# Kernel optimization log

Hardware: AMD Instinct MI355X
Metric: run time of the kernel (lower is better)

Reference implementation:

```python
import jax, jax.numpy as jnp
import numpy as np

BATCH, NUM_BSS, NUM_USERS, M, N = 32, 8, 32, 128, 4
LAGR_ITERS = 8
PSEUDOINV_SVAL_THRESH = 1e-12


def herm(a):
    return 0.5 * (a + jnp.swapaxes(a, -1, -2).conj())


def setup_inputs() -> dict:
    key = jax.random.key(0)
    ks = jax.random.split(key, 7)
    v_re = jax.random.normal(ks[0], (BATCH, NUM_USERS, M, N), jnp.float32)
    v_im = jax.random.normal(ks[1], (BATCH, NUM_USERS, M, N), jnp.float32)
    H_re = jax.random.normal(ks[2], (NUM_BSS, NUM_USERS, N, M), jnp.float32)
    H_im = jax.random.normal(ks[3], (NUM_BSS, NUM_USERS, N, M), jnp.float32)
    noise_pow = jax.random.uniform(ks[4], (BATCH, NUM_USERS), jnp.float32, 0.05, 1.0)
    rweights = jax.random.uniform(ks[5], (BATCH, NUM_USERS), jnp.float32, 0.1, 1.0)
    bss_pow = jnp.ones((BATCH, NUM_BSS), jnp.float32)
    assign = jax.random.randint(ks[6], (NUM_USERS,), 0, NUM_BSS).astype(jnp.int32)
    return {"v_re": v_re, "v_im": v_im, "H_re": H_re, "H_im": H_im,
            "noise_pow": noise_pow, "rweights": rweights, "bss_pow": bss_pow,
            "assign": assign}


def reference(v_re, v_im, H_re, H_im, noise_pow, rweights, bss_pow, assign):
    V = v_re + 1j * v_im          # [B,K,M,N] precoders
    H = H_re + 1j * H_im          # [C,K,N,M] channel BS c -> user k
    K = V.shape[1]
    C = H.shape[0]
    Ndim = V.shape[-1]
    eyeN = jnp.eye(Ndim, dtype=V.dtype)

    # Hg[j, i] = channel from assigned-BS-of-user-j to user i
    Hg = H[assign]                                    # [K,K,N,M]
    # downlink covariance per user i: noise*I + sum_j (H[bs_j,i] V_j)(.)^H
    HV = jnp.einsum('jinm,bjmp->bijnp', Hg, V)        # [B,Ki,Kj,N,N]
    cov = jnp.einsum('bijnp,bijqp->binq', HV, HV.conj())
    cov = herm(cov + noise_pow[..., None, None] * eyeN)
    icov = herm(jnp.linalg.inv(cov))                  # [B,K,N,N]

    idx = jnp.arange(K)
    Hd = Hg[idx, idx]                                 # [K,N,M] direct channels
    HdV = jnp.einsum('knm,bkmp->bknp', Hd, V)         # [B,K,N,N]
    u = jnp.einsum('bknq,bkqp->bknp', icov, HdV)      # receive filters
    w_inv = herm(eyeN - jnp.einsum('bkqn,bkqp->bknp', u.conj(), HdV))
    w = herm(jnp.linalg.inv(w_inv))                   # MSE weights (w_poly=None)
    uwu = herm(jnp.einsum('bknp,bkpq,bkrq->bknr', u, w, u.conj()))
    # v_tilde = H_ii^H u w * rate_weight
    vt = jnp.einsum('knm,bknp,bkpq->bkmq', Hd.conj(), u, w) * rweights[..., None, None]

    # uplink covariance per BS c: sum_k rw_k * H[c,k]^H uwu_k H[c,k]
    ul = herm(jnp.einsum('cknm,bkno,ckop,bk->bcmp', H.conj(), uwu, H, rweights))

    # aux per BS: sum over assigned users of v_tilde v_tilde^H
    Q = jnp.einsum('bkmn,bkpn->bkmp', vt, vt.conj())  # [B,K,M,M]
    aux = jnp.moveaxis(
        jax.ops.segment_sum(jnp.moveaxis(Q, 1, 0), assign, num_segments=C), 0, 1)  # [B,C,M,M]

    lam, E = jnp.linalg.eigh(ul)                      # [B,C,M], [B,C,M,M]
    lam = jnp.maximum(lam, 0.0)
    c = jnp.maximum(jnp.einsum('bcmi,bcmp,bcpi->bci', E.conj(), aux, E).real, 0.0)
    c = c / bss_pow[..., None]

    # solve sum_i c_i/(lam_i+mu)^2 = 1 for mu >= 0 by bisection in [0, sqrt(sum c)]
    hi = jnp.sqrt(jnp.sum(c, -1))
    lo = jnp.zeros_like(hi)
    for _ in range(LAGR_ITERS):
        mid = 0.5 * (lo + hi)
        f = jnp.sum(c / jnp.square(lam + mid[..., None] + 1e-20), -1)
        gt = f > 1.0
        lo = jnp.where(gt, mid, lo)
        hi = jnp.where(gt, hi, mid)
    mu = jnp.maximum(0.5 * (lo + hi), 0.0)            # [B,C]

    # pseudo-inverse of loaded UL covariance via its eigendecomposition
    lam_l = lam + mu[..., None]
    lam_l = jnp.where(lam_l < PSEUDOINV_SVAL_THRESH, 1e12, lam_l)
    inv_aug = herm(jnp.einsum('bcmi,bci,bcni->bcmn', E, 1.0 / lam_l, E.conj()))

    # v update: v_k = inv_aug[assign_k] @ v_tilde_k
    v_out = jnp.einsum('bkmp,bkpn->bkmn', inv_aug[:, assign], vt)  # [B,K,M,N]
    return v_out
```

## Files before the change

### kernel.cpp

```cpp
#include <hip/hip_runtime.h>

#define B_ 32
#define C_ 8
#define K_ 32
#define NCMAX 96
#define BSTR 129

__device__ __forceinline__ float2 cmul(float2 a, float2 b) {
  return make_float2(a.x*b.x - a.y*b.y, a.x*b.y + a.y*b.x);
}
__device__ __forceinline__ float2 cmulc(float2 a, float2 b) {
  return make_float2(a.x*b.x + a.y*b.y, a.y*b.x - a.x*b.y);
}
__device__ __forceinline__ float2 cadd(float2 a, float2 b){ return make_float2(a.x+b.x, a.y+b.y); }
__device__ __forceinline__ float2 csub(float2 a, float2 b){ return make_float2(a.x-b.x, a.y-b.y); }
__device__ __forceinline__ int SK(int r){ return r + ((r >> 3) << 1); }

__device__ void herm4_inv(float2 a[4][4], float2 out[4][4]) {
  float idg[4];
  for (int j = 0; j < 4; ++j) {
    float d = sqrtf(fmaxf(a[j][j].x, 1e-30f));
    float id = 1.f / d;
    idg[j] = id;
    a[j][j] = make_float2(d, 0.f);
    for (int r = j+1; r < 4; ++r) { a[r][j].x *= id; a[r][j].y *= id; }
    for (int c = j+1; c < 4; ++c)
      for (int r = c; r < 4; ++r)
        a[r][c] = csub(a[r][c], cmulc(a[r][j], a[c][j]));
  }
  float2 li[4][4];
  for (int j = 0; j < 4; ++j) {
    li[j][j] = make_float2(idg[j], 0.f);
    for (int r = j+1; r < 4; ++r) {
      float2 s = make_float2(0.f, 0.f);
      for (int d = j; d < r; ++d) s = cadd(s, cmul(a[r][d], li[d][j]));
      li[r][j] = make_float2(-s.x*idg[r], -s.y*idg[r]);
    }
  }
  for (int p = 0; p < 4; ++p)
    for (int q = 0; q < 4; ++q) {
      float2 s = make_float2(0.f, 0.f);
      for (int d = (p > q ? p : q); d < 4; ++d)
        s = cadd(s, cmulc(li[d][q], li[d][p]));
      out[p][q] = s;
    }
}

__global__ __launch_bounds__(512, 1) void k_fused(
    const float* __restrict__ v_re, const float* __restrict__ v_im,
    const float* __restrict__ H_re, const float* __restrict__ H_im,
    const float* __restrict__ noise_pow, const float* __restrict__ rweights,
    const float* __restrict__ bss_pow, const int* __restrict__ assign_g,
    void* __restrict__ outp, int omode)
{
  const int t = threadIdx.x;
  const int lane = t & 63, wid = t >> 6;
  const int blk = blockIdx.x;
  const int b = blk >> 3, c = blk & 7;
  const int tm = t >> 4, tp = t & 15;
  const int rbase = tm * 4, cbase = tp * 8;

  __shared__ __align__(16) float2 Bs[NCMAX * BSTR];
  __shared__ __align__(16) float2 Arena[4224];
  __shared__ __align__(16) float2 Vp[16 * 128];
  __shared__ __align__(16) float2 pS[1024];
  __shared__ __align__(16) float2 colS[160];
  __shared__ __align__(16) float2 pvS[160];
  __shared__ __align__(16) float2 tauS[128];
  __shared__ float dS[128], eS[128], cpS[128];
  __shared__ float red[8];
  __shared__ int asg[K_], ulist[K_], nc_s;

  float2* Wall = pS;
  float2* uwS  = pS + 512;
  float2* covS = Arena + 2576;
  float2* HdVS = Arena + 3088;
  float2* Hs   = Arena;
  float2* Ys   = Arena + 520;
  float2* Tsc  = Arena;

  if (t < K_) asg[t] = assign_g[t];
  if (t == 0) {
    int n2 = 0;
    for (int k = 0; k < K_; ++k) if (assign_g[k] == c) ulist[n2++] = k;
    nc_s = n2;
  }
  {
    const int k = t >> 4, n = (t >> 2) & 3, q = t & 3;
    covS[t] = make_float2((n == q) ? noise_pow[b*K_ + k] : 0.f, 0.f);
  }
  __syncthreads();
  const int nc = nc_s;
  if (nc == 0) return;
  const int cols = 4 * nc;
  const int passes = (cols + 31) >> 5;

  {
    const int pn = t >> 2, qt = t & 3;
    const int kk = pn >> 2, nn = pn & 3;
    float2* Tb0 = Arena + 1552;
    float2* Tb1 = Arena + 2064;
    for (int j = 0; j < K_; j += 2) {
      #pragma unroll
      for (int bf = 0; bf < 2; ++bf) {
        const int vb = (b*K_ + j + bf) * 512;
        Arena[bf*776 + (t >> 2)*6 + (t & 3) + (t >> 7)*2] =
            make_float2(v_re[vb + t], v_im[vb + t]);
      }
      __syncthreads();
      float2 rr[2][4];
      #pragma unroll
      for (int bf = 0; bf < 2; ++bf) {
        const float2* Vq = Arena + bf*776 + qt*2;
        const int hb = ((asg[j + bf]*K_ + kk)*4 + nn) * 128;
        float2 a0 = {0,0}, a1 = {0,0}, a2 = {0,0}, a3 = {0,0};
        for (int m4 = qt*32; m4 < qt*32 + 32; m4 += 4) {
          const float4 hre = *(const float4*)&H_re[hb + m4];
          const float4 him = *(const float4*)&H_im[hb + m4];
          const float hx[4] = {hre.x, hre.y, hre.z, hre.w};
          const float hy[4] = {him.x, him.y, him.z, him.w};
          #pragma unroll
          for (int i2 = 0; i2 < 4; ++i2) {
            const float4 v01 = *(const float4*)&Vq[(m4 + i2)*6];
            const float4 v23 = *(const float4*)&Vq[(m4 + i2)*6 + 2];
            a0.x += hx[i2]*v01.x - hy[i2]*v01.y; a0.y += hx[i2]*v01.y + hy[i2]*v01.x;
            a1.x += hx[i2]*v01.z - hy[i2]*v01.w; a1.y += hx[i2]*v01.w + hy[i2]*v01.z;
            a2.x += hx[i2]*v23.x - hy[i2]*v23.y; a2.y += hx[i2]*v23.y + hy[i2]*v23.x;
            a3.x += hx[i2]*v23.z - hy[i2]*v23.w; a3.y += hx[i2]*v23.w + hy[i2]*v23.z;
          }
        }
        rr[bf][0] = a0; rr[bf][1] = a1; rr[bf][2] = a2; rr[bf][3] = a3;
      }
      #pragma unroll
      for (int o = 1; o <= 2; o <<= 1) {
        #pragma unroll
        for (int bf = 0; bf < 2; ++bf)
          #pragma unroll
          for (int p = 0; p < 4; ++p) {
            rr[bf][p].x += __shfl_xor(rr[bf][p].x, o, 64);
            rr[bf][p].y += __shfl_xor(rr[bf][p].y, o, 64);
          }
      }
      if (qt == 0) {
        #pragma unroll
        for (int p = 0; p < 4; ++p) {
          Tb0[pn*4 + p] = rr[0][p];
          Tb1[pn*4 + p] = rr[1][p];
        }
      }
      __syncthreads();
      {
        const int k2 = t >> 4, n2 = (t >> 2) & 3, q2 = t & 3;
        float2 acc = covS[t];
        #pragma unroll
        for (int p = 0; p < 4; ++p)
          acc = cadd(acc, cmulc(Tb0[(k2*4 + n2)*4 + p], Tb0[(k2*4 + q2)*4 + p]));
        #pragma unroll
        for (int p = 0; p < 4; ++p)
          acc = cadd(acc, cmulc(Tb1[(k2*4 + n2)*4 + p], Tb1[(k2*4 + q2)*4 + p]));
        covS[t] = acc;
        if (k2 == j)     HdVS[k2*16 + n2*4 + q2] = Tb0[(k2*4 + n2)*4 + q2];
        if (k2 == j + 1) HdVS[k2*16 + n2*4 + q2] = Tb1[(k2*4 + n2)*4 + q2];
      }
      __syncthreads();
    }
  }

  if (t < K_) {
    const int k = t;
    float2 a[4][4], ic[4][4], hv[4][4], u[4][4], wi[4][4], w[4][4], uw[4][4], W[4][4];
    const float rwk = rweights[b*K_ + k];
    for (int r = 0; r < 4; ++r)
      for (int c2 = 0; c2 < 4; ++c2) a[r][c2] = covS[k*16 + r*4 + c2];
    herm4_inv(a, ic);
    for (int r = 0; r < 4; ++r)
      for (int c2 = 0; c2 < 4; ++c2) hv[r][c2] = HdVS[k*16 + r*4 + c2];
    for (int n = 0; n < 4; ++n)
      for (int p = 0; p < 4; ++p) {
        float2 s = {0,0};
        for (int q = 0; q < 4; ++q) s = cadd(s, cmul(ic[n][q], hv[q][p]));
        u[n][p] = s;
      }
    for (int n = 0; n < 4; ++n)
      for (int p = 0; p < 4; ++p) {
        float2 s = make_float2((n == p) ? 1.f : 0.f, 0.f);
        for (int q = 0; q < 4; ++q) s = csub(s, cmulc(hv[q][p], u[q][n]));
        wi[n][p] = s;
      }
    herm4_inv(wi, w);
    for (int n = 0; n < 4; ++n)
      for (int q = 0; q < 4; ++q) {
        float2 s = {0,0};
        for (int p = 0; p < 4; ++p) s = cadd(s, cmul(u[n][p], w[p][q]));
        uw[n][q] = s;
      }
    for (int n = 0; n < 4; ++n)
      for (int r = 0; r < 4; ++r) {
        float2 s = {0,0};
        for (int q = 0; q < 4; ++q) s = cadd(s, cmulc(uw[n][q], u[r][q]));
        W[n][r] = make_float2(s.x * rwk, s.y * rwk);
      }
    for (int n = 0; n < 4; ++n)
      for (int r = n; r < 4; ++r) {
        float2 x1 = W[n][r], x2 = W[r][n];
        float2 hm = make_float2(0.5f*(x1.x + x2.x), 0.5f*(x1.y - x2.y));
        W[n][r] = hm; W[r][n] = make_float2(hm.x, -hm.y);
      }
    for (int idx = 0; idx < 16; ++idx) {
      uwS[k*16 + idx]  = uw[idx >> 2][idx & 3];
      Wall[k*16 + idx] = W[idx >> 2][idx & 3];
    }
  }
  __syncthreads();

  float trp = 0.f;
  #pragma unroll
  for (int q = 0; q < 8; ++q) {
    const int col = tp + 16*q;
    const int slot = col >> 2, qn = col & 3;
    if (slot < nc) {
      const int k = ulist[slot];
      const float rwk = rweights[b*K_ + k];
      const int hb = (c*K_ + k) * 512;
      float2 acc0 = {0,0}, acc1 = {0,0}, acc2 = {0,0}, acc3 = {0,0};
      #pragma unroll
      for (int n = 0; n < 4; ++n) {
        const float2 uwv = uwS[k*16 + n*4 + qn];
        const float4 hre = *(const float4*)&H_re[hb + n*128 + rbase];
        const float4 him = *(const float4*)&H_im[hb + n*128 + rbase];
        acc0 = cadd(acc0, cmulc(uwv, make_float2(hre.x, him.x)));
        acc1 = cadd(acc1, cmulc(uwv, make_float2(hre.y, him.y)));
        acc2 = cadd(acc2, cmulc(uwv, make_float2(hre.z, him.z)));
        acc3 = cadd(acc3, cmulc(uwv, make_float2(hre.w, him.w)));
      }
      acc0.x *= rwk; acc0.y *= rwk; acc1.x *= rwk; acc1.y *= rwk;
      acc2.x *= rwk; acc2.y *= rwk; acc3.x *= rwk; acc3.y *= rwk;
      Bs[col*BSTR + rbase]     = acc0;
      Bs[col*BSTR + rbase + 1] = acc1;
      Bs[col*BSTR + rbase + 2] = acc2;
      Bs[col*BSTR + rbase + 3] = acc3;
      trp += acc0.x*acc0.x + acc0.y*acc0.y + acc1.x*acc1.x + acc1.y*acc1.y
           + acc2.x*acc2.x + acc2.y*acc2.y + acc3.x*acc3.x + acc3.y*acc3.y;
    }
  }
  #pragma unroll
  for (int o = 32; o >= 1; o >>= 1) trp += __shfl_xor(trp, o, 64);
  if (lane == 0) red[wid] = trp;
  __syncthreads();
  const float inv_bss = 1.f / bss_pow[b*C_ + c];
  float hi = sqrtf((red[0] + red[1] + red[2] + red[3] +
                    red[4] + red[5] + red[6] + red[7]) * inv_bss);
  float lo = 0.f;

  float2 Areg[4][8];
  #pragma unroll
  for (int j = 0; j < 4; ++j)
    #pragma unroll
    for (int cc = 0; cc < 8; ++cc) Areg[j][cc] = make_float2(0.f, 0.f);
  __syncthreads();
  for (int k = 0; k < K_; ++k) {
    const int hb = (c*K_ + k) * 512;
    Hs[(t >> 7)*130 + (t & 127)] = make_float2(H_re[hb + t], H_im[hb + t]);
    __syncthreads();
    {
      const int n = t >> 7, p = t & 127;
      float2 y = {0,0};
      #pragma unroll
      for (int o = 0; o < 4; ++o) y = cadd(y, cmul(Wall[k*16 + n*4 + o], Hs[o*130 + p]));
      Ys[n*160 + p + ((p >> 3) << 1)] = y;
    }
    __syncthreads();
    #pragma unroll
    for (int n = 0; n < 4; ++n) {
      float2 h[4], y[8];
      {
        const float4 ha = *(const float4*)&Hs[n*130 + rbase];
        const float4 hc = *(const float4*)&Hs[n*130 + rbase + 2];
        h[0] = make_float2(ha.x, ha.y); h[1] = make_float2(ha.z, ha.w);
        h[2] = make_float2(hc.x, hc.y); h[3] = make_float2(hc.z, hc.w);
        const float2* yb = &Ys[n*160 + tp*10];
        #pragma unroll
        for (int a2 = 0; a2 < 8; a2 += 2) {
          const float4 y4 = *(const float4*)&yb[a2];
          y[a2] = make_float2(y4.x, y4.y); y[a2+1] = make_float2(y4.z, y4.w);
        }
      }
      #pragma unroll
      for (int j = 0; j < 4; ++j)
        #pragma unroll
        for (int cc = 0; cc < 8; ++cc) {
          Areg[j][cc].x += h[j].x*y[cc].x + h[j].y*y[cc].y;
          Areg[j][cc].y += h[j].x*y[cc].y - h[j].y*y[cc].x;
        }
    }
    __syncthreads();
  }

  if (tp == 0) {
    #pragma unroll
    for (int j = 0; j < 4; ++j) colS[SK(rbase + j)] = Areg[j][0];
  }
  __syncthreads();

  #pragma unroll 1
  for (int i = 0; i < 127; ++i) {
    float2 vr[4], vc[8], tau, sc;
    const int slot = (i & 15) << 7;
    {
      const float2 x0 = colS[SK(lane)], x1 = colS[SK(lane + 64)];
      float sig = 0.f;
      if (lane >= i + 2)      sig += x0.x*x0.x + x0.y*x0.y;
      if (lane + 64 >= i + 2) sig += x1.x*x1.x + x1.y*x1.y;
      #pragma unroll
      for (int o = 32; o >= 1; o >>= 1) sig += __shfl_xor(sig, o, 64);
      const float2 al = colS[SK(i + 1)];
      float beta;
      if (sig <= 1e-30f && fabsf(al.y) <= 1e-30f) {
        beta = al.x; tau = make_float2(0.f, 0.f); sc = make_float2(0.f, 0.f);
      } else {
        const float mag = sqrtf(al.x*al.x + al.y*al.y + sig);
        beta = (al.x >= 0.f) ? -mag : mag;
        const float ib = 1.f / beta;
        tau = make_float2((beta - al.x) * ib, -al.y * ib);
        const float dx = al.x - beta, dy = al.y;
        const float dn = 1.f / (dx*dx + dy*dy);
        sc = make_float2(dx*dn, -dy*dn);
      }
      if (t == 0) { eS[i] = beta; tauS[i] = tau; }
      #pragma unroll
      for (int j = 0; j < 4; ++j) {
        const int r = rbase + j;
        const float2 x = colS[SK(r)];
        vr[j] = (r <= i) ? make_float2(0.f, 0.f)
              : (r == i + 1 ? make_float2(1.f, 0.f) : cmul(x, sc));
      }
      {
        const int cb = SK(cbase);
        const float4 c01 = *(const float4*)&colS[cb];
        const float4 c23 = *(const float4*)&colS[cb + 2];
        const float4 c45 = *(const float4*)&colS[cb + 4];
        const float4 c67 = *(const float4*)&colS[cb + 6];
        const float2 cx[8] = { make_float2(c01.x,c01.y), make_float2(c01.z,c01.w),
                               make_float2(c23.x,c23.y), make_float2(c23.z,c23.w),
                               make_float2(c45.x,c45.y), make_float2(c45.z,c45.w),
                               make_float2(c67.x,c67.y), make_float2(c67.z,c67.w) };
        #pragma unroll
        for (int cc = 0; cc < 8; ++cc) {
          const int r = cbase + cc;
          vc[cc] = (r <= i) ? make_float2(0.f, 0.f)
                 : (r == i + 1 ? make_float2(1.f, 0.f) : cmul(cx[cc], sc));
        }
      }
      if (tp == 0) {
        #pragma unroll
        for (int j = 0; j < 4; ++j) Vp[slot + rbase + j] = vr[j];
      }
      float2 part[4];
      #pragma unroll
      for (int j = 0; j < 4; ++j) {
        float2 s = cmul(Areg[j][0], vc[0]);
        #pragma unroll
        for (int cc = 1; cc < 8; ++cc) s = cadd(s, cmul(Areg[j][cc], vc[cc]));
        part[j] = s;
      }
      #pragma unroll
      for (int o = 1; o <= 8; o <<= 1) {
        #pragma unroll
        for (int j = 0; j < 4; ++j) {
          part[j].x += __shfl_xor(part[j].x, o, 64);
          part[j].y += __shfl_xor(part[j].y, o, 64);
        }
      }
      #pragma unroll
      for (int j = 0; j < 4; ++j) if (tp == j) pvS[SK(rbase + j)] = part[j];
    }
    __syncthreads();

    {
      float2 p0 = make_float2(0.f, 0.f), p1 = make_float2(0.f, 0.f);
      if (lane > i)      p0 = cmul(tau, pvS[SK(lane)]);
      if (lane + 64 > i) p1 = cmul(tau, pvS[SK(lane + 64)]);
      const float2 v0 = Vp[slot + lane];
      const float2 v1 = Vp[slot + lane + 64];
      float2 d0 = cadd(cmulc(p0, v0), cmulc(p1, v1));
      #pragma unroll
      for (int o = 32; o >= 1; o >>= 1) {
        d0.x += __shfl_xor(d0.x, o, 64);
        d0.y += __shfl_xor(d0.y, o, 64);
      }
      const float alr = -0.5f * (tau.x*d0.x + tau.y*d0.y);
      float2 wr[4];
      #pragma unroll
      for (int j = 0; j < 4; ++j) {
        const int r = rbase + j;
        float2 p = (r > i) ? cmul(tau, pvS[SK(r)]) : make_float2(0.f, 0.f);
        wr[j] = make_float2(p.x + alr*vr[j].x, p.y + alr*vr[j].y);
      }
      #pragma unroll
      for (int cc = 0; cc < 8; ++cc) {
        const int r = cbase + cc;
        float2 p = (r > i) ? cmul(tau, pvS[SK(r)]) : make_float2(0.f, 0.f);
        const float2 wcv = make_float2(p.x + alr*vc[cc].x, p.y + alr*vc[cc].y);
        #pragma unroll
        for (int j = 0; j < 4; ++j)
          Areg[j][cc] = csub(Areg[j][cc], cadd(cmulc(vr[j], wcv), cmulc(wr[j], vc[cc])));
      }
      if (tp == (i >> 3)) {
        #pragma unroll
        for (int cc = 0; cc < 8; ++cc) if (cc == (i & 7)) {
          #pragma unroll
          for (int j = 0; j < 4; ++j) if (rbase + j >= i + 1) Areg[j][cc] = vr[j];
        }
      }
      if (tp == ((i + 1) >> 3)) {
        #pragma unroll
        for (int cc = 0; cc < 8; ++cc) if (cc == ((i + 1) & 7)) {
          #pragma unroll
          for (int j = 0; j < 4; ++j) colS[SK(rbase + j)] = Areg[j][cc];
        }
      }
    }
    __syncthreads();

    if ((i & 15) == 15 || i == 126) {
      const int p0i = i & ~15;
      const int smax = i - p0i;
      for (int base = 0; base < cols; base += 32) {
        float2 z0[4], z1[4];
        bool act[4];
        #pragma unroll
        for (int qq = 0; qq < 4; ++qq) {
          const int col = base + wid + 8*qq;
          act[qq] = (col < cols);
          const int cc2 = act[qq] ? col : 0;
          z0[qq] = Bs[cc2*BSTR + lane];
          z1[qq] = Bs[cc2*BSTR + lane + 64];
        }
        for (int s = 0; s <= smax; ++s) {
          const float2 tv = tauS[p0i + s];
          const float2 tc = make_float2(tv.x, -tv.y);
          const float2 v0 = Vp[(s << 7) + lane];
          const float2 v1 = Vp[(s << 7) + lane + 64];
          float2 d[4];
          #pragma unroll
          for (int qq = 0; qq < 4; ++qq)
            d[qq] = cadd(cmulc(z0[qq], v0), cmulc(z1[qq], v1));
          #pragma unroll
          for (int o = 32; o >= 1; o >>= 1) {
            #pragma unroll
            for (int qq = 0; qq < 4; ++qq) {
              d[qq].x += __shfl_xor(d[qq].x, o, 64);
              d[qq].y += __shfl_xor(d[qq].y, o, 64);
            }
          }
          #pragma unroll
          for (int qq = 0; qq < 4; ++qq) {
            const float2 td = cmul(tc, d[qq]);
            z0[qq] = csub(z0[qq], cmul(td, v0));
            z1[qq] = csub(z1[qq], cmul(td, v1));
          }
        }
        #pragma unroll
        for (int qq = 0; qq < 4; ++qq) if (act[qq]) {
          const int col = base + wid + 8*qq;
          Bs[col*BSTR + lane]      = z0[qq];
          Bs[col*BSTR + lane + 64] = z1[qq];
        }
      }
      __syncthreads();
    }
  }

  #pragma unroll
  for (int j = 0; j < 4; ++j) {
    const int r = rbase + j;
    if (tp == (r >> 3)) {
      #pragma unroll
      for (int cc = 0; cc < 8; ++cc) if (cc == (r & 7)) dS[r] = Areg[j][cc].x;
    }
  }
  __syncthreads();

  if (wid == 0) {
    for (int it = 0; it <= 8; ++it) {
      const float mu = 0.5f * (lo + hi);
      float fsum = 0.f;
      for (int p = 0; p < passes; ++p) {
        const int colg = 32*p + (lane & 31);
        const bool act = (lane < 32) && (colg < cols);
        float2* Bcol = Bs + colg*BSTR;
        float m = dS[0] + mu;
        float im = 1.f / m;
        float2 g = act ? Bcol[0] : make_float2(0.f, 0.f);
        g.x *= im; g.y *= im;
        if (act) Tsc[lane] = g;
        float cp = eS[0] * im;
        if (lane == 0) cpS[0] = cp;
        for (int r = 1; r < 128; ++r) {
          const float e0 = eS[r-1];
          m = dS[r] + mu - e0 * cp;
          im = 1.f / m;
          float2 gr = act ? Bcol[r] : make_float2(0.f, 0.f);
          gr.x = (gr.x - e0 * g.x) * im;
          gr.y = (gr.y - e0 * g.y) * im;
          g = gr;
          if (act) Tsc[r*33 + lane] = gr;
          if (r < 127) { cp = eS[r] * im; if (lane == 0) cpS[r] = cp; }
        }
        float2 z = g;
        float acc = z.x*z.x + z.y*z.y;
        if (it == 8 && act) Bcol[127] = z;
        for (int r = 126; r >= 0; --r) {
          const float cpr = cpS[r];
          const float2 gp = act ? Tsc[r*33 + lane] : make_float2(0.f, 0.f);
          z.x = gp.x - cpr * z.x;
          z.y = gp.y - cpr * z.y;
          acc += z.x*z.x + z.y*z.y;
          if (it == 8 && act) Bcol[r] = z;
        }
        if (act) fsum += acc;
      }
      if (it < 8) {
        #pragma unroll
        for (int o = 32; o >= 1; o >>= 1) fsum += __shfl_xor(fsum, o, 64);
        const float f = fsum * inv_bss;
        if (f > 1.0f) lo = mu; else hi = mu;
      }
    }
  }
  __syncthreads();

  for (int base = 0; base < cols; base += 32) {
    float2 z0[4], z1[4];
    bool act[4];
    #pragma unroll
    for (int qq = 0; qq < 4; ++qq) {
      const int col = base + wid + 8*qq;
      act[qq] = (col < cols);
      const int cc2 = act[qq] ? col : 0;
      z0[qq] = Bs[cc2*BSTR + lane];
      z1[qq] = Bs[cc2*BSTR + lane + 64];
    }
    for (int P = 7; P >= 0; --P) {
      const int p0i = P * 16;
      const int smax = (P == 7) ? 14 : 15;
      __syncthreads();
      if (tp == 2*P) {
        #pragma unroll
        for (int s = 0; s < 8; ++s) {
          const int ii = p0i + s;
          #pragma unroll
          for (int j = 0; j < 4; ++j) {
            const int r = rbase + j;
            Vp[(s << 7) + r] = (r >= ii + 1) ? Areg[j][s] : make_float2(0.f, 0.f);
          }
        }
      }
      if (tp == 2*P + 1) {
        #pragma unroll
        for (int s = 8; s < 16; ++s) {
          if (s > smax) continue;
          const int ii = p0i + s;
          #pragma unroll
          for (int j = 0; j < 4; ++j) {
            const int r = rbase + j;
            Vp[(s << 7) + r] = (r >= ii + 1) ? Areg[j][s - 8] : make_float2(0.f, 0.f);
          }
        }
      }
      __syncthreads();
      for (int s = smax; s >= 0; --s) {
        const float2 tv = tauS[p0i + s];
        const float2 v0 = Vp[(s << 7) + lane];
        const float2 v1 = Vp[(s << 7) + lane + 64];
        float2 d[4];
        #pragma unroll
        for (int qq = 0; qq < 4; ++qq)
          d[qq] = cadd(cmulc(z0[qq], v0), cmulc(z1[qq], v1));
        #pragma unroll
        for (int o = 32; o >= 1; o >>= 1) {
          #pragma unroll
          for (int qq = 0; qq < 4; ++qq) {
            d[qq].x += __shfl_xor(d[qq].x, o, 64);
            d[qq].y += __shfl_xor(d[qq].y, o, 64);
          }
        }
        #pragma unroll
        for (int qq = 0; qq < 4; ++qq) {
          const float2 td = cmul(tv, d[qq]);
          z0[qq] = csub(z0[qq], cmul(td, v0));
          z1[qq] = csub(z1[qq], cmul(td, v1));
        }
      }
    }
    #pragma unroll
    for (int qq = 0; qq < 4; ++qq) if (act[qq]) {
      const int col = base + wid + 8*qq;
      const int slotc = col >> 2, qn = col & 3;
      const int k = ulist[slotc];
      const size_t obase = (size_t)(b*K_ + k) * 512;
      const size_t oe0 = obase + (size_t)lane*4 + qn;
      const size_t oe1 = obase + (size_t)(lane + 64)*4 + qn;
      if (omode == 0) {
        ((float2*)outp)[oe0] = z0[qq];
        ((float2*)outp)[oe1] = z1[qq];
      } else {
        ((float*)outp)[oe0] = z0[qq].x;
        ((float*)outp)[oe1] = z1[qq].x;
      }
    }
  }
}

extern "C" void kernel_launch(void* const* d_in, const int* in_sizes, int n_in,
                              void* d_out, int out_size, void* d_ws, size_t ws_size,
                              hipStream_t stream)
{
  (void)in_sizes; (void)n_in; (void)d_ws; (void)ws_size;
  const float* v_re   = (const float*)d_in[0];
  const float* v_im   = (const float*)d_in[1];
  const float* H_re   = (const float*)d_in[2];
  const float* H_im   = (const float*)d_in[3];
  const float* noise  = (const float*)d_in[4];
  const float* rw     = (const float*)d_in[5];
  const float* bss    = (const float*)d_in[6];
  const int*   assign = (const int*)d_in[7];

  const int omode = (out_size == B_*K_*128*4) ? 1 : 0;

  hipLaunchKernelGGL(k_fused, dim3(B_*C_), dim3(512), 0, stream,
                     v_re, v_im, H_re, H_im, noise, rw, bss, assign, d_out, omode);
}
```

Baseline: 1.472 ms.

## Apply Householder reflections to B in registers during tridiagonalization

The right-hand-side matrix B now lives in per-thread registers (Bv) and each Householder reflector is applied to it on every step through a cross-thread partial-product reduction in shared memory. This replaces the blocked every-16-steps application that went through a stored Vp panel and wavefront shuffles. The w vector is built once by wave 0 and read from shared memory instead of being recomputed per thread. The A accumulation loop is also moved earlier and processes two users per sync. The costs are extra register pressure, an added reduction and barrier on every iteration, and Vp now aliasing Arena.

Result: faster. 1.354 ms (-8.0%).

```diff
diff --git a/kernel.cpp b/kernel.cpp
--- a/kernel.cpp
+++ b/kernel.cpp
@@ -60,12 +60,13 @@
   const int tm = t >> 4, tp = t & 15;
   const int rbase = tm * 4, cbase = tp * 8;
 
-  __shared__ __align__(16) float2 Bs[NCMAX * BSTR];
+  __shared__ __align__(16) float2 BsL[NCMAX * BSTR];
   __shared__ __align__(16) float2 Arena[4224];
-  __shared__ __align__(16) float2 Vp[16 * 128];
   __shared__ __align__(16) float2 pS[1024];
+  __shared__ __align__(16) float2 dBS2[256];
+  __shared__ __align__(16) float2 wS[160];
   __shared__ __align__(16) float2 colS[160];
-  __shared__ __align__(16) float2 pvS[160];
+  __shared__ __align__(16) float2 pvS[128];
   __shared__ __align__(16) float2 tauS[128];
   __shared__ float dS[128], eS[128], cpS[128];
   __shared__ float red[8];
@@ -75,9 +76,9 @@
   float2* uwS  = pS + 512;
   float2* covS = Arena + 2576;
   float2* HdVS = Arena + 3088;
-  float2* Hs   = Arena;
-  float2* Ys   = Arena + 520;
+  float2* Pd   = Arena;
   float2* Tsc  = Arena;
+  float2* Vp   = Arena;
 
   if (t < K_) asg[t] = assign_g[t];
   if (t == 0) {
@@ -93,6 +94,7 @@
   const int nc = nc_s;
   if (nc == 0) return;
   const int cols = 4 * nc;
+  const int qmax = (cols + 15) >> 4;
   const int passes = (cols + 31) >> 5;
 
   {
@@ -213,6 +215,71 @@
   }
   __syncthreads();
 
+  float2 Areg[4][8];
+  #pragma unroll
+  for (int j = 0; j < 4; ++j)
+    #pragma unroll
+    for (int cc = 0; cc < 8; ++cc) Areg[j][cc] = make_float2(0.f, 0.f);
+  for (int k = 0; k < K_; k += 2) {
+    #pragma unroll
+    for (int bf = 0; bf < 2; ++bf) {
+      const int hb = (c*K_ + k + bf) * 512;
+      Arena[bf*520 + (t >> 7)*130 + (t & 127)] = make_float2(H_re[hb + t], H_im[hb + t]);
+    }
+    __syncthreads();
+    #pragma unroll
+    for (int bf = 0; bf < 2; ++bf) {
+      const int n = t >> 7, p = t & 127;
+      const float2* HsB = Arena + bf*520;
+      const int kb = (k + bf)*16 + n*4;
+      float2 y = {0,0};
+      #pragma unroll
+      for (int o = 0; o < 4; ++o) y = cadd(y, cmul(Wall[kb + o], HsB[o*130 + p]));
+      Arena[1040 + bf*640 + n*160 + p + ((p >> 3) << 1)] = y;
+    }
+    __syncthreads();
+    #pragma unroll
+    for (int bf = 0; bf < 2; ++bf) {
+      const float2* HsB = Arena + bf*520;
+      const float2* YsB = Arena + 1040 + bf*640;
+      #pragma unroll
+      for (int n = 0; n < 4; ++n) {
+        const float4 ha = *(const float4*)&HsB[n*130 + rbase];
+        const float4 hc = *(const float4*)&HsB[n*130 + rbase + 2];
+        const float2 h0 = make_float2(ha.x, ha.y), h1 = make_float2(ha.z, ha.w);
+        const float2 h2 = make_float2(hc.x, hc.y), h3 = make_float2(hc.z, hc.w);
+        const float2* yb = &YsB[n*160 + tp*10];
+        #pragma unroll
+        for (int hq = 0; hq < 2; ++hq) {
+          float2 y[4];
+          #pragma unroll
+          for (int a2 = 0; a2 < 4; a2 += 2) {
+            const float4 y4 = *(const float4*)&yb[hq*4 + a2];
+            y[a2] = make_float2(y4.x, y4.y); y[a2+1] = make_float2(y4.z, y4.w);
+          }
+          #pragma unroll
+          for (int c4 = 0; c4 < 4; ++c4) {
+            const int cc = hq*4 + c4;
+            Areg[0][cc].x += h0.x*y[c4].x + h0.y*y[c4].y;
+            Areg[0][cc].y += h0.x*y[c4].y - h0.y*y[c4].x;
+            Areg[1][cc].x += h1.x*y[c4].x + h1.y*y[c4].y;
+            Areg[1][cc].y += h1.x*y[c4].y - h1.y*y[c4].x;
+            Areg[2][cc].x += h2.x*y[c4].x + h2.y*y[c4].y;
+            Areg[2][cc].y += h2.x*y[c4].y - h2.y*y[c4].x;
+            Areg[3][cc].x += h3.x*y[c4].x + h3.y*y[c4].y;
+            Areg[3][cc].y += h3.x*y[c4].y - h3.y*y[c4].x;
+          }
+        }
+      }
+    }
+    __syncthreads();
+  }
+
+  float2 Bv[4][8];
+  #pragma unroll
+  for (int j = 0; j < 4; ++j)
+    #pragma unroll
+    for (int q = 0; q < 8; ++q) Bv[j][q] = make_float2(0.f, 0.f);
   float trp = 0.f;
   #pragma unroll
   for (int q = 0; q < 8; ++q) {
@@ -235,10 +302,7 @@
       }
       acc0.x *= rwk; acc0.y *= rwk; acc1.x *= rwk; acc1.y *= rwk;
       acc2.x *= rwk; acc2.y *= rwk; acc3.x *= rwk; acc3.y *= rwk;
-      Bs[col*BSTR + rbase]     = acc0;
-      Bs[col*BSTR + rbase + 1] = acc1;
-      Bs[col*BSTR + rbase + 2] = acc2;
-      Bs[col*BSTR + rbase + 3] = acc3;
+      Bv[0][q] = acc0; Bv[1][q] = acc1; Bv[2][q] = acc2; Bv[3][q] = acc3;
       trp += acc0.x*acc0.x + acc0.y*acc0.y + acc1.x*acc1.x + acc1.y*acc1.y
            + acc2.x*acc2.x + acc2.y*acc2.y + acc3.x*acc3.x + acc3.y*acc3.y;
     }
@@ -252,50 +316,6 @@
                     red[4] + red[5] + red[6] + red[7]) * inv_bss);
   float lo = 0.f;
 
-  float2 Areg[4][8];
-  #pragma unroll
-  for (int j = 0; j < 4; ++j)
-    #pragma unroll
-    for (int cc = 0; cc < 8; ++cc) Areg[j][cc] = make_float2(0.f, 0.f);
-  __syncthreads();
-  for (int k = 0; k < K_; ++k) {
-    const int hb = (c*K_ + k) * 512;
-    Hs[(t >> 7)*130 + (t & 127)] = make_float2(H_re[hb + t], H_im[hb + t]);
-    __syncthreads();
-    {
-      const int n = t >> 7, p = t & 127;
-      float2 y = {0,0};
-      #pragma unroll
-      for (int o = 0; o < 4; ++o) y = cadd(y, cmul(Wall[k*16 + n*4 + o], Hs[o*130 + p]));
-      Ys[n*160 + p + ((p >> 3) << 1)] = y;
-    }
-    __syncthreads();
-    #pragma unroll
-    for (int n = 0; n < 4; ++n) {
-      float2 h[4], y[8];
-      {
-        const float4 ha = *(const float4*)&Hs[n*130 + rbase];
-        const float4 hc = *(const float4*)&Hs[n*130 + rbase + 2];
-        h[0] = make_float2(ha.x, ha.y); h[1] = make_float2(ha.z, ha.w);
-        h[2] = make_float2(hc.x, hc.y); h[3] = make_float2(hc.z, hc.w);
-        const float2* yb = &Ys[n*160 + tp*10];
-        #pragma unroll
-        for (int a2 = 0; a2 < 8; a2 += 2) {
-          const float4 y4 = *(const float4*)&yb[a2];
-          y[a2] = make_float2(y4.x, y4.y); y[a2+1] = make_float2(y4.z, y4.w);
-        }
-      }
-      #pragma unroll
-      for (int j = 0; j < 4; ++j)
-        #pragma unroll
-        for (int cc = 0; cc < 8; ++cc) {
-          Areg[j][cc].x += h[j].x*y[cc].x + h[j].y*y[cc].y;
-          Areg[j][cc].y += h[j].x*y[cc].y - h[j].y*y[cc].x;
-        }
-    }
-    __syncthreads();
-  }
-
   if (tp == 0) {
     #pragma unroll
     for (int j = 0; j < 4; ++j) colS[SK(rbase + j)] = Areg[j][0];
@@ -305,7 +325,6 @@
   #pragma unroll 1
   for (int i = 0; i < 127; ++i) {
     float2 vr[4], vc[8], tau, sc;
-    const int slot = (i & 15) << 7;
     {
       const float2 x0 = colS[SK(lane)], x1 = colS[SK(lane + 64)];
       float sig = 0.f;
@@ -351,10 +370,8 @@
                  : (r == i + 1 ? make_float2(1.f, 0.f) : cmul(cx[cc], sc));
         }
       }
-      if (tp == 0) {
-        #pragma unroll
-        for (int j = 0; j < 4; ++j) Vp[slot + rbase + j] = vr[j];
-      }
+    }
+    {
       float2 part[4];
       #pragma unroll
       for (int j = 0; j < 4; ++j) {
@@ -372,16 +389,28 @@
         }
       }
       #pragma unroll
-      for (int j = 0; j < 4; ++j) if (tp == j) pvS[SK(rbase + j)] = part[j];
+      for (int j = 0; j < 4; ++j) if (tp == j) pvS[rbase + j] = part[j];
+      #pragma unroll
+      for (int q = 0; q < 8; ++q) {
+        if (q >= qmax) continue;
+        float2 s = {0.f, 0.f};
+        #pragma unroll
+        for (int j = 0; j < 4; ++j) s = cadd(s, cmulc(Bv[j][q], vr[j]));
+        Pd[tm*130 + tp + 16*q] = s;
+      }
     }
     __syncthreads();
 
-    {
-      float2 p0 = make_float2(0.f, 0.f), p1 = make_float2(0.f, 0.f);
-      if (lane > i)      p0 = cmul(tau, pvS[SK(lane)]);
-      if (lane + 64 > i) p1 = cmul(tau, pvS[SK(lane + 64)]);
-      const float2 v0 = Vp[slot + lane];
-      const float2 v1 = Vp[slot + lane + 64];
+    if (wid == 0) {
+      float2 p0 = {0.f,0.f}, p1 = {0.f,0.f};
+      if (lane > i)      p0 = cmul(tau, pvS[lane]);
+      if (lane + 64 > i) p1 = cmul(tau, pvS[lane + 64]);
+      float2 v0, v1;
+      v0 = (lane <= i) ? make_float2(0.f,0.f)
+         : (lane == i + 1 ? make_float2(1.f,0.f) : cmul(colS[SK(lane)], sc));
+      { const int r1 = lane + 64;
+        v1 = (r1 <= i) ? make_float2(0.f,0.f)
+           : (r1 == i + 1 ? make_float2(1.f,0.f) : cmul(colS[SK(r1)], sc)); }
       float2 d0 = cadd(cmulc(p0, v0), cmulc(p1, v1));
       #pragma unroll
       for (int o = 32; o >= 1; o >>= 1) {
@@ -389,21 +418,45 @@
         d0.y += __shfl_xor(d0.y, o, 64);
       }
       const float alr = -0.5f * (tau.x*d0.x + tau.y*d0.y);
-      float2 wr[4];
-      #pragma unroll
-      for (int j = 0; j < 4; ++j) {
-        const int r = rbase + j;
-        float2 p = (r > i) ? cmul(tau, pvS[SK(r)]) : make_float2(0.f, 0.f);
-        wr[j] = make_float2(p.x + alr*vr[j].x, p.y + alr*vr[j].y);
-      }
-      #pragma unroll
-      for (int cc = 0; cc < 8; ++cc) {
-        const int r = cbase + cc;
-        float2 p = (r > i) ? cmul(tau, pvS[SK(r)]) : make_float2(0.f, 0.f);
-        const float2 wcv = make_float2(p.x + alr*vc[cc].x, p.y + alr*vc[cc].y);
-        #pragma unroll
-        for (int j = 0; j < 4; ++j)
-          Areg[j][cc] = csub(Areg[j][cc], cadd(cmulc(vr[j], wcv), cmulc(wr[j], vc[cc])));
+      wS[SK(lane)]      = cadd(p0, make_float2(alr*v0.x, alr*v0.y));
+      wS[SK(lane + 64)] = cadd(p1, make_float2(alr*v1.x, alr*v1.y));
+    } else if (t < 320) {
+      const int col = (t - 64) & 127;
+      const int half = (t - 64) >> 7;
+      float2 s = {0.f, 0.f};
+      #pragma unroll
+      for (int g = 0; g < 16; ++g) s = cadd(s, Pd[(half*16 + g)*130 + col]);
+      dBS2[half*128 + col] = s;
+    }
+    __syncthreads();
+
+    {
+      float2 wr[4], wc[8];
+      #pragma unroll
+      for (int j = 0; j < 4; ++j) wr[j] = wS[SK(rbase + j)];
+      {
+        const int cb = SK(cbase);
+        const float4 w01 = *(const float4*)&wS[cb];
+        const float4 w23 = *(const float4*)&wS[cb + 2];
+        const float4 w45 = *(const float4*)&wS[cb + 4];
+        const float4 w67 = *(const float4*)&wS[cb + 6];
+        wc[0] = make_float2(w01.x,w01.y); wc[1] = make_float2(w01.z,w01.w);
+        wc[2] = make_float2(w23.x,w23.y); wc[3] = make_float2(w23.z,w23.w);
+        wc[4] = make_float2(w45.x,w45.y); wc[5] = make_float2(w45.z,w45.w);
+        wc[6] = make_float2(w67.x,w67.y); wc[7] = make_float2(w67.z,w67.w);
+      }
+      #pragma unroll
+      for (int j = 0; j < 4; ++j)
+        #pragma unroll
+        for (int cc = 0; cc < 8; ++cc)
+          Areg[j][cc] = csub(Areg[j][cc], cadd(cmulc(vr[j], wc[cc]), cmulc(wr[j], vc[cc])));
+      const float2 tauc = make_float2(tau.x, -tau.y);
+      #pragma unroll
+      for (int q = 0; q < 8; ++q) {
+        if (q >= qmax) continue;
+        const float2 dBt = cmul(tauc, cadd(dBS2[tp + 16*q], dBS2[128 + tp + 16*q]));
+        #pragma unroll
+        for (int j = 0; j < 4; ++j) Bv[j][q] = csub(Bv[j][q], cmul(dBt, vr[j]));
       }
       if (tp == (i >> 3)) {
         #pragma unroll
@@ -421,62 +474,22 @@
       }
     }
     __syncthreads();
-
-    if ((i & 15) == 15 || i == 126) {
-      const int p0i = i & ~15;
-      const int smax = i - p0i;
-      for (int base = 0; base < cols; base += 32) {
-        float2 z0[4], z1[4];
-        bool act[4];
-        #pragma unroll
-        for (int qq = 0; qq < 4; ++qq) {
-          const int col = base + wid + 8*qq;
-          act[qq] = (col < cols);
-          const int cc2 = act[qq] ? col : 0;
-          z0[qq] = Bs[cc2*BSTR + lane];
-          z1[qq] = Bs[cc2*BSTR + lane + 64];
-        }
-        for (int s = 0; s <= smax; ++s) {
-          const float2 tv = tauS[p0i + s];
-          const float2 tc = make_float2(tv.x, -tv.y);
-          const float2 v0 = Vp[(s << 7) + lane];
-          const float2 v1 = Vp[(s << 7) + lane + 64];
-          float2 d[4];
-          #pragma unroll
-          for (int qq = 0; qq < 4; ++qq)
-            d[qq] = cadd(cmulc(z0[qq], v0), cmulc(z1[qq], v1));
-          #pragma unroll
-          for (int o = 32; o >= 1; o >>= 1) {
-            #pragma unroll
-            for (int qq = 0; qq < 4; ++qq) {
-              d[qq].x += __shfl_xor(d[qq].x, o, 64);
-              d[qq].y += __shfl_xor(d[qq].y, o, 64);
-            }
-          }
-          #pragma unroll
-          for (int qq = 0; qq < 4; ++qq) {
-            const float2 td = cmul(tc, d[qq]);
-            z0[qq] = csub(z0[qq], cmul(td, v0));
-            z1[qq] = csub(z1[qq], cmul(td, v1));
-          }
-        }
-        #pragma unroll
-        for (int qq = 0; qq < 4; ++qq) if (act[qq]) {
-          const int col = base + wid + 8*qq;
-          Bs[col*BSTR + lane]      = z0[qq];
-          Bs[col*BSTR + lane + 64] = z1[qq];
-        }
-      }
-      __syncthreads();
-    }
-  }
-
+  }
+
+  if (tp == (tm >> 1)) {
+    const int co = (tm & 1) * 4;
+    #pragma unroll
+    for (int j = 0; j < 4; ++j)
+      #pragma unroll
+      for (int cc = 0; cc < 8; ++cc)
+        if (cc == co + j) dS[rbase + j] = Areg[j][cc].x;
+  }
   #pragma unroll
-  for (int j = 0; j < 4; ++j) {
-    const int r = rbase + j;
-    if (tp == (r >> 3)) {
-      #pragma unroll
-      for (int cc = 0; cc < 8; ++cc) if (cc == (r & 7)) dS[r] = Areg[j][cc].x;
+  for (int q = 0; q < 8; ++q) {
+    const int col = tp + 16*q;
+    if ((col >> 2) < nc) {
+      #pragma unroll
+      for (int j = 0; j < 4; ++j) BsL[col*BSTR + rbase + j] = Bv[j][q];
     }
   }
   __syncthreads();
@@ -488,7 +501,7 @@
       for (int p = 0; p < passes; ++p) {
         const int colg = 32*p + (lane & 31);
         const bool act = (lane < 32) && (colg < cols);
-        float2* Bcol = Bs + colg*BSTR;
+        float2* Bcol = BsL + colg*BSTR;
         float m = dS[0] + mu;
         float im = 1.f / m;
         float2 g = act ? Bcol[0] : make_float2(0.f, 0.f);
@@ -538,8 +551,8 @@
       const int col = base + wid + 8*qq;
       act[qq] = (col < cols);
       const int cc2 = act[qq] ? col : 0;
-      z0[qq] = Bs[cc2*BSTR + lane];
-      z1[qq] = Bs[cc2*BSTR + lane + 64];
+      z0[qq] = BsL[cc2*BSTR + lane];
+      z1[qq] = BsL[cc2*BSTR + lane + 64];
     }
     for (int P = 7; P >= 0; --P) {
       const int p0i = P * 16;
```
